# Kernel tuning notes

Measured on AMD Instinct MI355X. Metric: run time of the kernel, lower is better.

Reference implementation:

```python
import jax, jax.numpy as jnp
import numpy as np

WS = 16  # window_size

def _conv1x1(x, w, b):
    # x: [n,c,h,w], w: [out,in], b: [out]
    return jnp.einsum('nchw,oc->nohw', x, w) + b[None, :, None, None]

def _se_attention(x, w1, b1, w2, b2):
    # global avg pool -> conv -> relu -> conv -> sigmoid; returns [n,C,1,1]
    p = x.mean(axis=(2, 3), keepdims=True)
    h = jax.nn.relu(_conv1x1(p, w1, b1))
    return jax.nn.sigmoid(_conv1x1(h, w2, b2))

def setup_inputs() -> dict:
    key = jax.random.key(0)
    ks = jax.random.split(key, 13)
    B, C, H, W = 8, 96, 256, 256
    Cr = C // 3
    s = 0.02
    return {
        'x': jax.random.normal(ks[0], (B, C, H, W), jnp.float32),
        'w_real': jax.random.normal(ks[1], (C, C), jnp.float32) * s,
        'b_real': jnp.zeros((C,), jnp.float32),
        'w_imag': jax.random.normal(ks[2], (C, C), jnp.float32) * s,
        'b_imag': jnp.zeros((C,), jnp.float32),
        'car_w1': jax.random.normal(ks[3], (Cr, C), jnp.float32) * s,
        'car_b1': jnp.zeros((Cr,), jnp.float32),
        'car_w2': jax.random.normal(ks[4], (C, Cr), jnp.float32) * s,
        'car_b2': jnp.zeros((C,), jnp.float32),
        'cai_w1': jax.random.normal(ks[5], (Cr, C), jnp.float32) * s,
        'cai_b1': jnp.zeros((Cr,), jnp.float32),
        'cai_w2': jax.random.normal(ks[6], (C, Cr), jnp.float32) * s,
        'cai_b2': jnp.zeros((C,), jnp.float32),
    }

def reference(x, w_real, b_real, w_imag, b_imag,
              car_w1, car_b1, car_w2, car_b2,
              cai_w1, cai_b1, cai_w2, cai_b2):
    B, C, H, W = x.shape
    nH, nW = H // WS, W // WS
    # window partition: [B,C,H,W] -> [B*nH*nW, C, WS, WS]
    xw = x.reshape(B, C, nH, WS, nW, WS)
    xw = xw.transpose(0, 2, 4, 1, 3, 5).reshape(-1, C, WS, WS)
    # 2D FFT per window, ortho norm
    x_fft = jnp.fft.fft2(xw, norm='ortho')
    real_conv = _conv1x1(jnp.real(x_fft), w_real, b_real)
    imag_conv = _conv1x1(jnp.imag(x_fft), w_imag, b_imag)
    real_att = _se_attention(real_conv, car_w1, car_b1, car_w2, car_b2)
    imag_att = _se_attention(imag_conv, cai_w1, cai_b1, cai_w2, cai_b2)
    real_conv = real_conv * (1.0 + real_att)
    imag_conv = imag_conv * (1.0 + imag_att)
    x_fft_enh = jax.lax.complex(real_conv, imag_conv)
    x_ifft = jnp.real(jnp.fft.ifft2(x_fft_enh, norm='ortho'))
    # window merge: [B*nH*nW, C, WS, WS] -> [B,C,H,W]
    out = x_ifft.reshape(B, nH, nW, C, WS, WS)
    out = out.transpose(0, 3, 1, 4, 2, 5).reshape(B, C, H, W)
    return out
```

## Files before the change

### kernel.cpp

```cpp
#include <hip/hip_runtime.h>
#include <hip/hip_bf16.h>
#include <math.h>

#define NWIN 2048

typedef __bf16 v8bf __attribute__((ext_vector_type(8)));
typedef __bf16 v2bf __attribute__((ext_vector_type(2)));
typedef float  v4f  __attribute__((ext_vector_type(4)));
typedef unsigned int v4u __attribute__((ext_vector_type(4)));

__global__ __launch_bounds__(128) void se_alpha_kernel(
    const float* __restrict__ x,
    const float* __restrict__ w_real, const float* __restrict__ b_real,
    const float* __restrict__ car_w1, const float* __restrict__ car_b1,
    const float* __restrict__ car_w2, const float* __restrict__ car_b2,
    const float* __restrict__ b_imag,
    const float* __restrict__ cai_w1, const float* __restrict__ cai_b1,
    const float* __restrict__ cai_w2, const float* __restrict__ cai_b2,
    float* __restrict__ alpha, float* __restrict__ beta)
{
    __shared__ float wr_s[96 * 97];
    __shared__ float vec_s[96];
    __shared__ float pr_s[96];
    __shared__ float h1_s[32];
    const int t = threadIdx.x;
    const int n = blockIdx.x;

    if (n < NWIN) {
        const int b = n >> 8, wh = (n >> 4) & 15, ww = n & 15;
        for (int idx = t; idx < 96 * 96; idx += 128) {
            int o = idx / 96;
            int c = idx - o * 96;
            wr_s[o * 97 + c] = w_real[idx];
        }
        if (t < 96)
            vec_s[t] = x[(((size_t)(b * 96 + t)) * 256 + wh * 16) * 256 + ww * 16];
        __syncthreads();
        if (t < 96) {
            float acc = 0.f;
            #pragma unroll 8
            for (int c = 0; c < 96; ++c) acc += wr_s[t * 97 + c] * vec_s[c];
            pr_s[t] = acc * (1.0f / 16.0f) + b_real[t];
        }
        __syncthreads();
        if (t < 32) {
            float acc = car_b1[t];
            for (int o = 0; o < 96; ++o) acc += car_w1[t * 96 + o] * pr_s[o];
            h1_s[t] = fmaxf(acc, 0.f);
        }
        __syncthreads();
        if (t < 96) {
            float acc = car_b2[t];
            for (int j = 0; j < 32; ++j) acc += car_w2[t * 32 + j] * h1_s[j];
            alpha[n * 96 + t] = 1.f + 1.f / (1.f + __expf(-acc));
        }
    } else {
        if (t < 32) {
            float acc = cai_b1[t];
            for (int o = 0; o < 96; ++o) acc += cai_w1[t * 96 + o] * b_imag[o];
            h1_s[t] = fmaxf(acc, 0.f);
        }
        __syncthreads();
        if (t < 96) {
            float acc = cai_b2[t];
            for (int j = 0; j < 32; ++j) acc += cai_w2[t * 32 + j] * h1_s[j];
            beta[t] = 1.f + 1.f / (1.f + __expf(-acc));
        }
    }
}

__global__ __launch_bounds__(1024, 4) void wfca_main_kernel(
    const float* __restrict__ x,
    const float* __restrict__ w_real, const float* __restrict__ w_imag,
    const float* __restrict__ b_real,
    const float* __restrict__ alpha, const float* __restrict__ beta,
    float* __restrict__ out)
{
    __shared__ __bf16 wr_s[96 * 104];
    __shared__ __bf16 wi_s[96 * 104];
    __shared__ __bf16 x_lds[2][256 * 40];

    const int t    = threadIdx.x;
    const int blk  = blockIdx.x;
    const int b    = blk >> 5;
    const int wh   = (blk >> 1) & 15;
    const int ww0  = (blk & 1) * 8;

    const int lane = t & 63;
    const int l16  = lane & 15;
    const int quad = lane >> 4;
    const int wv   = t >> 6;

    const int sw  = t & 15;
    const int scp = (t >> 4) & 15;
    const int hq  = t >> 8;

    const float* xb = x + (((size_t)(b * 96)) << 16) + (size_t)(wh * 16) * 256;

    float st0[4], st1[4];

    auto stage_issue = [&](int win_, int k_) {
        const float* xp = xb + (((size_t)(k_ * 32 + 2 * scp)) << 16)
                             + (ww0 + win_) * 16 + sw;
        #pragma unroll
        for (int r = 0; r < 4; ++r) {
            int h = hq * 4 + r;
            st0[r] = xp[h * 256];
            st1[r] = xp[h * 256 + 65536];
        }
    };
    auto stage_write = [&](int bufsel) {
        #pragma unroll
        for (int r = 0; r < 4; ++r) {
            int h = hq * 4 + r;
            v2bf pk;
            pk[0] = (__bf16)st0[r];
            pk[1] = (__bf16)st1[r];
            *(v2bf*)&x_lds[bufsel][(h * 16 + sw) * 40 + 2 * scp] = pk;
        }
    };

    stage_issue(0, 0);
    {
        float wrv[9], wiv[9], btv[9];
        #pragma unroll
        for (int r = 0; r < 9; ++r) {
            int idx = t + r * 1024;
            wrv[r] = w_real[idx];
            wiv[r] = w_imag[idx];
            btv[r] = beta[idx / 96];
        }
        #pragma unroll
        for (int r = 0; r < 9; ++r) {
            int idx = t + r * 1024;
            int o = idx / 96, c = idx - o * 96;
            wr_s[o * 104 + c] = (__bf16)(0.5f * wrv[r]);
            wi_s[o * 104 + c] = (__bf16)(0.5f * btv[r] * wiv[r]);
        }
    }
    stage_write(0);
    __syncthreads();

    v4f acc[6];
    int cur = 0;
    for (int win = 0; win < 8; ++win) {
        float af[6];
        #pragma unroll
        for (int n = 0; n < 6; ++n) {
            af[n] = alpha[(size_t)(blk * 8 + win) * 96 + n * 16 + l16];
            acc[n] = v4f{0.f, 0.f, 0.f, 0.f};
        }
        for (int k = 0; k < 3; ++k) {
            const bool last = (win == 7 && k == 2);
            if (!last) stage_issue(k == 2 ? win + 1 : win, k == 2 ? 0 : k + 1);

            const __bf16* xl = x_lds[cur];
            v8bf a_x = *(const v8bf*)&xl[(wv * 16 + l16) * 40 + quad * 8];
            const int hf = (16 - wv) & 15, wf = (16 - l16) & 15;
            v8bf a_f = *(const v8bf*)&xl[(hf * 16 + wf) * 40 + quad * 8];
            v4u fu = __builtin_bit_cast(v4u, a_f);
            const v4u sm = {0x80008000u, 0x80008000u, 0x80008000u, 0x80008000u};
            v8bf a_fn = __builtin_bit_cast(v8bf, fu ^ sm);

            const int c0 = k * 32;
            #pragma unroll
            for (int n = 0; n < 6; ++n) {
                v8bf bwr = *(const v8bf*)&wr_s[(n * 16 + l16) * 104 + c0 + quad * 8];
                v8bf bwi = *(const v8bf*)&wi_s[(n * 16 + l16) * 104 + c0 + quad * 8];
                acc[n] = __builtin_amdgcn_mfma_f32_16x16x32_bf16(a_x,  bwi, acc[n], 0, 0, 0);
                acc[n] = __builtin_amdgcn_mfma_f32_16x16x32_bf16(a_fn, bwi, acc[n], 0, 0, 0);
                v4f utmp = __builtin_amdgcn_mfma_f32_16x16x32_bf16(
                               a_x, bwr, v4f{0.f, 0.f, 0.f, 0.f}, 0, 0, 0);
                utmp = __builtin_amdgcn_mfma_f32_16x16x32_bf16(a_f, bwr, utmp, 0, 0, 0);
                #pragma unroll
                for (int r = 0; r < 4; ++r) acc[n][r] += af[n] * utmp[r];
            }
            if (k == 2) {
                const int col = (ww0 + win) * 16;
                #pragma unroll
                for (int n = 0; n < 6; ++n) {
                    const int o = n * 16 + l16;
                    v4f v = acc[n];
                    if (wv == 0 && quad == 0) {
                        v[0] += 16.f * af[n] * b_real[o];
                    }
                    size_t idx = (((size_t)(b * 96 + o)) * 256 + wh * 16 + wv) * 256
                                 + col + quad * 4;
                    *(v4f*)(out + idx) = v;
                }
            }
            if (!last) stage_write(cur ^ 1);
            __syncthreads();
            cur ^= 1;
        }
    }
}

extern "C" void kernel_launch(void* const* d_in, const int* in_sizes, int n_in,
                              void* d_out, int out_size, void* d_ws, size_t ws_size,
                              hipStream_t stream) {
    const float* x      = (const float*)d_in[0];
    const float* w_real = (const float*)d_in[1];
    const float* b_real = (const float*)d_in[2];
    const float* w_imag = (const float*)d_in[3];
    const float* b_imag = (const float*)d_in[4];
    const float* car_w1 = (const float*)d_in[5];
    const float* car_b1 = (const float*)d_in[6];
    const float* car_w2 = (const float*)d_in[7];
    const float* car_b2 = (const float*)d_in[8];
    const float* cai_w1 = (const float*)d_in[9];
    const float* cai_b1 = (const float*)d_in[10];
    const float* cai_w2 = (const float*)d_in[11];
    const float* cai_b2 = (const float*)d_in[12];
    float* out = (float*)d_out;

    float* alpha = (float*)d_ws;
    float* beta  = alpha + NWIN * 96;

    se_alpha_kernel<<<NWIN + 1, 128, 0, stream>>>(
        x, w_real, b_real, car_w1, car_b1, car_w2, car_b2,
        b_imag, cai_w1, cai_b1, cai_w2, cai_b2, alpha, beta);

    wfca_main_kernel<<<256, 1024, 0, stream>>>(
        x, w_real, w_imag, b_real, alpha, beta, out);
}
```

Measured before the change: 441.5 us.

## Batch SE alpha over 16 windows per block and stage whole windows in LDS

The SE alpha kernel now processes a row of 16 windows per block, 129 blocks instead of 2049. The weight matrices are loaded into shared memory once per block rather than once per window, which removes the redundant weight traffic. The main kernel stages all 96 channels of a window at once into a larger LDS buffer and synchronises once per window instead of once per 32-channel chunk. This cuts barriers and lets global loads overlap with a full window of MFMA work, at the cost of more registers and more LDS, which may lower occupancy.

```diff
diff --git a/kernel.cpp b/kernel.cpp
--- a/kernel.cpp
+++ b/kernel.cpp
@@ -20,39 +20,62 @@
     float* __restrict__ alpha, float* __restrict__ beta)
 {
     __shared__ float wr_s[96 * 97];
-    __shared__ float vec_s[96];
-    __shared__ float pr_s[96];
-    __shared__ float h1_s[32];
+    __shared__ float w1_s[32 * 97];
+    __shared__ float w2_s[96 * 33];
+    __shared__ float x0_s[96 * 17];
+    __shared__ float pr_s[16 * 97];
+    __shared__ float h1_s[16 * 33];
     const int t = threadIdx.x;
-    const int n = blockIdx.x;
-
-    if (n < NWIN) {
-        const int b = n >> 8, wh = (n >> 4) & 15, ww = n & 15;
+    const int blkid = blockIdx.x;
+
+    if (blkid < 128) {
+        const int b = blkid >> 4, wh = blkid & 15;
         for (int idx = t; idx < 96 * 96; idx += 128) {
-            int o = idx / 96;
-            int c = idx - o * 96;
+            int o = idx / 96, c = idx - o * 96;
             wr_s[o * 97 + c] = w_real[idx];
         }
-        if (t < 96)
-            vec_s[t] = x[(((size_t)(b * 96 + t)) * 256 + wh * 16) * 256 + ww * 16];
-        __syncthreads();
-        if (t < 96) {
+        for (int idx = t; idx < 32 * 96; idx += 128) {
+            int j = idx / 96, c = idx - j * 96;
+            w1_s[j * 97 + c] = car_w1[idx];
+        }
+        for (int idx = t; idx < 96 * 32; idx += 128) {
+            int o = idx >> 5, j = idx & 31;
+            w2_s[o * 33 + j] = car_w2[idx];
+        }
+        for (int idx = t; idx < 96 * 16; idx += 128) {
+            int c = idx >> 4, w = idx & 15;
+            x0_s[c * 17 + w] = x[(((size_t)(b * 96 + c)) * 256 + wh * 16) * 256 + w * 16];
+        }
+        __syncthreads();
+        #pragma unroll
+        for (int i = 0; i < 12; ++i) {
+            int p = t + i * 128;
+            int o = p >> 4, w = p & 15;
             float acc = 0.f;
-            #pragma unroll 8
-            for (int c = 0; c < 96; ++c) acc += wr_s[t * 97 + c] * vec_s[c];
-            pr_s[t] = acc * (1.0f / 16.0f) + b_real[t];
-        }
-        __syncthreads();
-        if (t < 32) {
-            float acc = car_b1[t];
-            for (int o = 0; o < 96; ++o) acc += car_w1[t * 96 + o] * pr_s[o];
-            h1_s[t] = fmaxf(acc, 0.f);
-        }
-        __syncthreads();
-        if (t < 96) {
-            float acc = car_b2[t];
-            for (int j = 0; j < 32; ++j) acc += car_w2[t * 32 + j] * h1_s[j];
-            alpha[n * 96 + t] = 1.f + 1.f / (1.f + __expf(-acc));
+            #pragma unroll 4
+            for (int c = 0; c < 96; ++c) acc += wr_s[o * 97 + c] * x0_s[c * 17 + w];
+            pr_s[w * 97 + o] = acc * (1.0f / 16.0f) + b_real[o];
+        }
+        __syncthreads();
+        #pragma unroll
+        for (int i = 0; i < 4; ++i) {
+            int p = t + i * 128;
+            int j = p >> 4, w = p & 15;
+            float acc = car_b1[j];
+            #pragma unroll 4
+            for (int o = 0; o < 96; ++o) acc += w1_s[j * 97 + o] * pr_s[w * 97 + o];
+            h1_s[w * 33 + j] = fmaxf(acc, 0.f);
+        }
+        __syncthreads();
+        #pragma unroll
+        for (int i = 0; i < 12; ++i) {
+            int p = t + i * 128;
+            int o = p >> 4, w = p & 15;
+            float acc = car_b2[o];
+            #pragma unroll
+            for (int j = 0; j < 32; ++j) acc += w2_s[o * 33 + j] * h1_s[w * 33 + j];
+            int n = (blkid << 4) | w;
+            alpha[(size_t)n * 96 + o] = 1.f + 1.f / (1.f + __expf(-acc));
         }
     } else {
         if (t < 32) {
@@ -78,7 +101,7 @@
 {
     __shared__ __bf16 wr_s[96 * 104];
     __shared__ __bf16 wi_s[96 * 104];
-    __shared__ __bf16 x_lds[2][256 * 40];
+    __shared__ __bf16 x_lds[2][256 * 104];
 
     const int t    = threadIdx.x;
     const int blk  = blockIdx.x;
@@ -90,37 +113,40 @@
     const int l16  = lane & 15;
     const int quad = lane >> 4;
     const int wv   = t >> 6;
-
-    const int sw  = t & 15;
-    const int scp = (t >> 4) & 15;
-    const int hq  = t >> 8;
+    const int hf   = (16 - wv) & 15;
+    const int wf   = (16 - l16) & 15;
+
+    const int sw = t & 15;
+    const int g  = t >> 4;
 
     const float* xb = x + (((size_t)(b * 96)) << 16) + (size_t)(wh * 16) * 256;
 
-    float st0[4], st1[4];
-
-    auto stage_issue = [&](int win_, int k_) {
-        const float* xp = xb + (((size_t)(k_ * 32 + 2 * scp)) << 16)
-                             + (ww0 + win_) * 16 + sw;
-        #pragma unroll
-        for (int r = 0; r < 4; ++r) {
-            int h = hq * 4 + r;
-            st0[r] = xp[h * 256];
-            st1[r] = xp[h * 256 + 65536];
+    float st0[12], st1[12];
+
+    auto stage_issue = [&](int win_) {
+        const float* xp = xb + (ww0 + win_) * 16 + sw;
+        #pragma unroll
+        for (int i = 0; i < 12; ++i) {
+            int j = g * 12 + i;
+            int cp = j >> 4, h = j & 15;
+            const float* p = xp + (((size_t)(2 * cp)) << 16) + h * 256;
+            st0[i] = p[0];
+            st1[i] = p[65536];
         }
     };
     auto stage_write = [&](int bufsel) {
         #pragma unroll
-        for (int r = 0; r < 4; ++r) {
-            int h = hq * 4 + r;
+        for (int i = 0; i < 12; ++i) {
+            int j = g * 12 + i;
+            int cp = j >> 4, h = j & 15;
             v2bf pk;
-            pk[0] = (__bf16)st0[r];
-            pk[1] = (__bf16)st1[r];
-            *(v2bf*)&x_lds[bufsel][(h * 16 + sw) * 40 + 2 * scp] = pk;
+            pk[0] = (__bf16)st0[i];
+            pk[1] = (__bf16)st1[i];
+            *(v2bf*)&x_lds[bufsel][(h * 16 + sw) * 104 + 2 * cp] = pk;
         }
     };
 
-    stage_issue(0, 0);
+    stage_issue(0);
     {
         float wrv[9], wiv[9], btv[9];
         #pragma unroll
@@ -141,28 +167,29 @@
     stage_write(0);
     __syncthreads();
 
-    v4f acc[6];
     int cur = 0;
     for (int win = 0; win < 8; ++win) {
         float af[6];
         #pragma unroll
-        for (int n = 0; n < 6; ++n) {
+        for (int n = 0; n < 6; ++n)
             af[n] = alpha[(size_t)(blk * 8 + win) * 96 + n * 16 + l16];
-            acc[n] = v4f{0.f, 0.f, 0.f, 0.f};
-        }
+
+        if (win < 7) stage_issue(win + 1);
+
+        v4f acc[6];
+        #pragma unroll
+        for (int n = 0; n < 6; ++n) acc[n] = v4f{0.f, 0.f, 0.f, 0.f};
+
+        const __bf16* xl = x_lds[cur];
+        #pragma unroll
         for (int k = 0; k < 3; ++k) {
-            const bool last = (win == 7 && k == 2);
-            if (!last) stage_issue(k == 2 ? win + 1 : win, k == 2 ? 0 : k + 1);
-
-            const __bf16* xl = x_lds[cur];
-            v8bf a_x = *(const v8bf*)&xl[(wv * 16 + l16) * 40 + quad * 8];
-            const int hf = (16 - wv) & 15, wf = (16 - l16) & 15;
-            v8bf a_f = *(const v8bf*)&xl[(hf * 16 + wf) * 40 + quad * 8];
+            const int c0 = k * 32;
+            v8bf a_x = *(const v8bf*)&xl[(wv * 16 + l16) * 104 + c0 + quad * 8];
+            v8bf a_f = *(const v8bf*)&xl[(hf * 16 + wf) * 104 + c0 + quad * 8];
             v4u fu = __builtin_bit_cast(v4u, a_f);
             const v4u sm = {0x80008000u, 0x80008000u, 0x80008000u, 0x80008000u};
             v8bf a_fn = __builtin_bit_cast(v8bf, fu ^ sm);
 
-            const int c0 = k * 32;
             #pragma unroll
             for (int n = 0; n < 6; ++n) {
                 v8bf bwr = *(const v8bf*)&wr_s[(n * 16 + l16) * 104 + c0 + quad * 8];
@@ -175,21 +202,25 @@
                 #pragma unroll
                 for (int r = 0; r < 4; ++r) acc[n][r] += af[n] * utmp[r];
             }
-            if (k == 2) {
-                const int col = (ww0 + win) * 16;
-                #pragma unroll
-                for (int n = 0; n < 6; ++n) {
-                    const int o = n * 16 + l16;
-                    v4f v = acc[n];
-                    if (wv == 0 && quad == 0) {
-                        v[0] += 16.f * af[n] * b_real[o];
-                    }
-                    size_t idx = (((size_t)(b * 96 + o)) * 256 + wh * 16 + wv) * 256
-                                 + col + quad * 4;
-                    *(v4f*)(out + idx) = v;
+        }
+
+        {
+            const int col = (ww0 + win) * 16;
+            #pragma unroll
+            for (int n = 0; n < 6; ++n) {
+                const int o = n * 16 + l16;
+                v4f v = acc[n];
+                if (wv == 0 && quad == 0) {
+                    v[0] += 16.f * af[n] * b_real[o];
                 }
+                size_t idx = (((size_t)(b * 96 + o)) * 256 + wh * 16 + wv) * 256
+                             + col + quad * 4;
+                *(v4f*)(out + idx) = v;
             }
-            if (!last) stage_write(cur ^ 1);
+        }
+
+        if (win < 7) {
+            stage_write(cur ^ 1);
             __syncthreads();
             cur ^= 1;
         }
@@ -217,7 +248,7 @@
     float* alpha = (float*)d_ws;
     float* beta  = alpha + NWIN * 96;
 
-    se_alpha_kernel<<<NWIN + 1, 128, 0, stream>>>(
+    se_alpha_kernel<<<129, 128, 0, stream>>>(
         x, w_real, b_real, car_w1, car_b1, car_w2, car_b2,
         b_imag, cai_w1, cai_b1, cai_w2, cai_b2, alpha, beta);
 
```

Result: slower. 505.5 us (+14.5%).
